# Kernel optimization log

Hardware: AMD Instinct MI355X
Metric: run time of the kernel (lower is better)

Reference implementation:

```python
import jax, jax.numpy as jnp
import numpy as np

B, NL, C, H, W = 4, 2048, 128, 128, 128
N_PTS0, N_PTS1 = 32, 8
SCALE = N_PTS0 // N_PTS1  # MaxPool1d kernel/stride
FEATURE_DIM = 5
BN_EPS = 1e-5


def setup_inputs() -> dict:
    key = jax.random.key(0)
    ks = jax.random.split(key, 12)
    fm = jax.random.normal(ks[0], (B, C, H, W), dtype=jnp.float32)
    lines = jax.random.uniform(ks[1], (B, NL, 2, 2), dtype=jnp.float32) * 128.0
    P = C // 2
    s = 0.05
    return {
        "feature_map": fm,
        "lines": lines,
        # Bottleneck1D params (BatchNorm in eval mode: running_mean=0, running_var=1)
        "bn1_g": jnp.ones((C,), jnp.float32), "bn1_b": jnp.zeros((C,), jnp.float32),
        "conv1_w": jax.random.normal(ks[2], (P, C, 1), jnp.float32) * s,
        "conv1_b": jnp.zeros((P,), jnp.float32),
        "bn2_g": jnp.ones((P,), jnp.float32), "bn2_b": jnp.zeros((P,), jnp.float32),
        "conv2_w": jax.random.normal(ks[3], (P, P, 3), jnp.float32) * s,
        "conv2_b": jnp.zeros((P,), jnp.float32),
        "bn3_g": jnp.ones((P,), jnp.float32), "bn3_b": jnp.zeros((P,), jnp.float32),
        "conv3_w": jax.random.normal(ks[4], (C, P, 1), jnp.float32) * s,
        "conv3_b": jnp.zeros((C,), jnp.float32),
        # fc2: ReLU -> Linear(dim_loi*n_pts1 + 5, 4)
        "fc2_w": jax.random.normal(ks[5], (4, C * N_PTS1 + FEATURE_DIM), jnp.float32) * s,
        "fc2_b": jnp.zeros((4,), jnp.float32),
    }


def _bn(x, g, b):
    # eval-mode BatchNorm1d with running_mean=0, running_var=1
    return x * (g / jnp.sqrt(1.0 + BN_EPS))[None, :, None] + b[None, :, None]


def _conv1d(x, w, b, pad):
    y = jax.lax.conv_general_dilated(x, w, (1,), [(pad, pad)],
                                     dimension_numbers=("NCH", "OIH", "NCH"))
    return y + b[None, :, None]


def _loi_gather(fm, lines):
    # sample points along each line: [B, NL, N_PTS0, 2]
    lam = jnp.linspace(0.0, 1.0, N_PTS0, dtype=jnp.float32)[None, None, :, None]
    p = lines[:, :, 0:1, :] * lam + lines[:, :, 1:2, :] * (1.0 - lam) - 0.5
    p = p.reshape(B, -1, 2)                      # [B, NL*N_PTS0, 2]
    px, py = p[..., 0], p[..., 1]
    px0 = jnp.clip(jnp.floor(px), 0.0, 127.0)
    py0 = jnp.clip(jnp.floor(py), 0.0, 127.0)
    px1 = jnp.clip(px0 + 1.0, 0.0, 127.0)
    py1 = jnp.clip(py0 + 1.0, 0.0, 127.0)
    px0l, py0l = px0.astype(jnp.int32), py0.astype(jnp.int32)
    px1l, py1l = px1.astype(jnp.int32), py1.astype(jnp.int32)

    gather = jax.vmap(lambda f, yi, xi: f[:, yi, xi])  # [C, P] per image
    # weights exactly as in the torch source
    xp = (gather(fm, py0l, px0l) * ((px1 - px) * (py1 - py))[:, None, :]
          + gather(fm, py1l, px0l) * ((px - px0) * (py1 - py))[:, None, :]
          + gather(fm, py0l, px1l) * ((px1 - px) * (py - py0))[:, None, :]
          + gather(fm, py1l, px1l) * ((px - px0) * (py - py0))[:, None, :])
    # [B, C, NL*N_PTS0] -> [B*NL, C, N_PTS0]
    xp = xp.reshape(B, C, NL, N_PTS0).transpose(0, 2, 1, 3).reshape(B * NL, C, N_PTS0)
    return xp


def reference(feature_map, lines, bn1_g, bn1_b, conv1_w, conv1_b,
              bn2_g, bn2_b, conv2_w, conv2_b, bn3_g, bn3_b,
              conv3_w, conv3_b, fc2_w, fc2_b):
    xp = _loi_gather(feature_map, lines)               # [B*NL, C, N_PTS0]
    # MaxPool1d(SCALE, SCALE)
    x = xp.reshape(B * NL, C, N_PTS1, SCALE).max(axis=-1)
    # Bottleneck1D residual block
    y = jax.nn.relu(_bn(x, bn1_g, bn1_b))
    y = _conv1d(y, conv1_w, conv1_b, 0)
    y = jax.nn.relu(_bn(y, bn2_g, bn2_b))
    y = _conv1d(y, conv2_w, conv2_b, 1)
    y = jax.nn.relu(_bn(y, bn3_g, bn3_b))
    y = _conv1d(y, conv3_w, conv3_b, 0)
    x = x + y                                          # [B*NL, C, N_PTS1]
    # line geometry feature (use_cood=1, use_slop=1)
    xyu, xyv = lines[:, :, 0, :], lines[:, :, 1, :]
    u2v = jnp.sqrt(((xyu - xyv) ** 2).sum(-1, keepdims=True)).clip(min=1e-6)
    f = jnp.concatenate([xyu / 128.0, xyv / 128.0, u2v], axis=-1)
    f = f.reshape(B * NL, FEATURE_DIM)
    # concat + fc2 (ReLU -> Linear)
    x = jnp.concatenate([x.reshape(B * NL, C * N_PTS1), f], axis=1)
    logits = jax.nn.relu(x) @ fc2_w.T + fc2_b
    prob = jax.nn.softmax(logits, axis=1)
    return logits, prob
```

## Files before the change

### kernel.cpp

```cpp
#include <hip/hip_runtime.h>
#include <math.h>

#define BB 4
#define NLL 2048
#define CC 128
#define HH 128
#define WW 128
#define NPTS0 32
#define NPTS1 8
#define PP 64
#define FDIM 5
#define FCK (CC*NPTS1 + FDIM)
#define FCKP 1032

typedef __attribute__((ext_vector_type(8))) short bf16x8;
typedef __attribute__((ext_vector_type(4))) float f32x4;

__device__ __forceinline__ unsigned short f2bf(float f) {
    union { float f; unsigned u; } v; v.f = f;
    unsigned u = v.u;
    return (unsigned short)((u + 0x7fffu + ((u >> 16) & 1u)) >> 16);
}
__device__ __forceinline__ float bf2f(unsigned short s) {
    union { unsigned u; float f; } v; v.u = ((unsigned)s) << 16;
    return v.f;
}

__global__ __launch_bounds__(256)
void transpose_prep(const float* __restrict__ fm, const float* __restrict__ w1,
                    const float* __restrict__ w2, const float* __restrict__ w3,
                    const float* __restrict__ fcw,
                    unsigned short* __restrict__ fmT,
                    unsigned short* __restrict__ W1b,
                    unsigned short* __restrict__ W2b,
                    unsigned short* __restrict__ W3b,
                    float* __restrict__ fcwP) {
    const int t = threadIdx.x;
    if (blockIdx.x >= 512) {
        int gid = (blockIdx.x - 512) * 256 + t;
        for (int e = gid; e < 32800; e += 4096) {
            if (e < 8192) {
                W1b[e] = f2bf(w1[e]);
            } else if (e < 20480) {
                int g = e - 8192;
                int tt = g >> 12, r = g & 4095;
                int p = r >> 6, q = r & 63;
                W2b[tt * 4096 + p * 64 + q] = f2bf(w2[p * 192 + q * 3 + tt]);
            } else if (e < 28672) {
                int g = e - 20480;
                W3b[g] = f2bf(w3[g]);
            } else {
                int g = e - 28672;
                int o = g / FCKP, r = g - o * FCKP;
                fcwP[g] = (r < FCK) ? fcw[o * FCK + r] : 0.0f;
            }
        }
        return;
    }
    __shared__ unsigned short tile[2][128 * 72];
    const int by = blockIdx.x;
    const int b = by >> 7, y = by & 127;
    const float* src = fm + ((size_t)b * CC) * (HH * WW) + (size_t)y * WW;
    const int x4 = (t & 31) * 4;
    const int xh = x4 >> 6, xl = x4 & 63;
    #pragma unroll
    for (int i = 0; i < 16; ++i) {
        int r = (t >> 5) + 8 * i;
        float4 v = *(const float4*)&src[(size_t)r * (HH * WW) + x4];
        ushort4 u;
        u.x = f2bf(v.x); u.y = f2bf(v.y); u.z = f2bf(v.z); u.w = f2bf(v.w);
        *(ushort4*)&tile[xh][r * 72 + (xl ^ (r & 28))] = u;
    }
    __syncthreads();
    const int c4 = (t & 31) * 4;
    #pragma unroll
    for (int h = 0; h < 2; ++h) {
        unsigned short* dst = fmT + ((size_t)by * WW + h * 64) * CC;
        #pragma unroll
        for (int i = 0; i < 8; ++i) {
            int x = (t >> 5) + 8 * i;
            ushort4 u;
            u.x = tile[h][(c4 + 0) * 72 + (x ^ ((c4 + 0) & 28))];
            u.y = tile[h][(c4 + 1) * 72 + (x ^ ((c4 + 1) & 28))];
            u.z = tile[h][(c4 + 2) * 72 + (x ^ ((c4 + 2) & 28))];
            u.w = tile[h][(c4 + 3) * 72 + (x ^ ((c4 + 3) & 28))];
            *(ushort4*)&dst[(size_t)x * CC + c4] = u;
        }
    }
}

__global__ __launch_bounds__(256, 8)
void line_mfma(const unsigned short* __restrict__ fmT,
               const float* __restrict__ lines,
               const float* __restrict__ bn1_g, const float* __restrict__ bn1_b,
               const unsigned short* __restrict__ W1b, const float* __restrict__ b1,
               const float* __restrict__ bn2_g, const float* __restrict__ bn2_b,
               const unsigned short* __restrict__ W2b, const float* __restrict__ b2,
               const float* __restrict__ bn3_g, const float* __restrict__ bn3_b,
               const unsigned short* __restrict__ W3b, const float* __restrict__ b3,
               const float* __restrict__ fcwP,  const float* __restrict__ fcb,
               float* __restrict__ out) {
    __shared__ int   s_oA[64], s_oB[64], s_oC[64], s_oD[64];
    __shared__ float s_wA[64], s_wB[64], s_wC[64], s_wD[64];
    __shared__ float s_xs[16 * 132];
    __shared__ unsigned short s_ybn[16 * 136];
    __shared__ unsigned short s_z1[2 * 10 * 72];
    __shared__ unsigned short s_z2[16 * 72];
    __shared__ float s_feat[2][8];
    __shared__ float s_red[4 * 8];

    const int bx  = blockIdx.x;
    const int L0  = bx * 2;
    const int b   = bx >> 10;
    const int tid = threadIdx.x;
    const int lane = tid & 63;
    const int wv   = tid >> 6;
    const int quad = lane >> 4;
    const int l16  = lane & 15;
    const float inv_s = 1.0f / sqrtf(1.0f + 1e-5f);

    if (tid < 64) {
        int line = tid >> 5, pt = tid & 31;
        const float* ln = lines + (size_t)(L0 + line) * 4;
        float lam = (float)pt * (1.0f / 31.0f);
        float om  = 1.0f - lam;
        float px = ln[0] * lam + ln[2] * om - 0.5f;
        float py = ln[1] * lam + ln[3] * om - 0.5f;
        float px0 = fminf(fmaxf(floorf(px), 0.0f), 127.0f);
        float py0 = fminf(fmaxf(floorf(py), 0.0f), 127.0f);
        float px1 = fminf(px0 + 1.0f, 127.0f);
        float py1 = fminf(py0 + 1.0f, 127.0f);
        int ix0 = (int)px0, ix1 = (int)px1, iy0 = (int)py0, iy1 = (int)py1;
        s_oA[tid] = (iy0 * WW + ix0) * CC;
        s_oB[tid] = (iy1 * WW + ix0) * CC;
        s_oC[tid] = (iy0 * WW + ix1) * CC;
        s_oD[tid] = (iy1 * WW + ix1) * CC;
        float ax = px1 - px, bxv = px - px0, ay = py1 - py, byv = py - py0;
        s_wA[tid] = ax  * ay;
        s_wB[tid] = bxv * ay;
        s_wC[tid] = ax  * byv;
        s_wD[tid] = bxv * byv;
    }
    if (tid >= 64 && tid < 66) {
        int line = tid - 64;
        const float* ln = lines + (size_t)(L0 + line) * 4;
        float ux = ln[0], uy = ln[1], vx = ln[2], vy = ln[3];
        float dx = ux - vx, dy = uy - vy;
        float d = fmaxf(sqrtf(dx * dx + dy * dy), 1e-6f);
        s_feat[line][0] = ux * (1.0f / 128.0f);
        s_feat[line][1] = uy * (1.0f / 128.0f);
        s_feat[line][2] = vx * (1.0f / 128.0f);
        s_feat[line][3] = vy * (1.0f / 128.0f);
        s_feat[line][4] = d;
    }
    if (tid < 128) {
        int line = tid >> 6, q = tid & 63;
        s_z1[line * 720 + 0 * 72 + q] = 0;
        s_z1[line * 720 + 9 * 72 + q] = 0;
    }
    __syncthreads();

    {
        int tl = tid >> 4;
        int line = tl >> 3, k = tl & 7;
        int c8 = (tid & 15) * 8;
        const unsigned short* base = fmT + (size_t)b * (HH * WW * CC) + c8;
        float acc[8];
        #pragma unroll
        for (int i = 0; i < 8; ++i) acc[i] = -INFINITY;
        #pragma unroll
        for (int j = 0; j < 4; ++j) {
            int pt = line * 32 + k * 4 + j;
            bf16x8 rA = *(const bf16x8*)(base + s_oA[pt]);
            bf16x8 rB = *(const bf16x8*)(base + s_oB[pt]);
            bf16x8 rC = *(const bf16x8*)(base + s_oC[pt]);
            bf16x8 rD = *(const bf16x8*)(base + s_oD[pt]);
            float wA = s_wA[pt], wB = s_wB[pt], wC = s_wC[pt], wD = s_wD[pt];
            #pragma unroll
            for (int i = 0; i < 8; ++i) {
                float v = wA * bf2f((unsigned short)rA[i])
                        + wB * bf2f((unsigned short)rB[i])
                        + wC * bf2f((unsigned short)rC[i])
                        + wD * bf2f((unsigned short)rD[i]);
                acc[i] = fmaxf(acc[i], v);
            }
        }
        float* xr = &s_xs[tl * 132 + c8];
        f32x4 lo = {acc[0], acc[1], acc[2], acc[3]};
        f32x4 hi = {acc[4], acc[5], acc[6], acc[7]};
        *(f32x4*)&xr[0] = lo;
        *(f32x4*)&xr[4] = hi;
        bf16x8 pack;
        #pragma unroll
        for (int i = 0; i < 8; ++i) {
            float v = fmaxf(acc[i] * (bn1_g[c8 + i] * inv_s) + bn1_b[c8 + i], 0.0f);
            pack[i] = (short)f2bf(v);
        }
        *(bf16x8*)&s_ybn[tl * 136 + c8] = pack;
    }
    __syncthreads();

    {
        int n0 = wv * 16;
        f32x4 acc = {0.f, 0.f, 0.f, 0.f};
        #pragma unroll
        for (int kc = 0; kc < 4; ++kc) {
            bf16x8 a = *(const bf16x8*)&s_ybn[l16 * 136 + kc * 32 + quad * 8];
            bf16x8 bf = *(const bf16x8*)(W1b + (n0 + l16) * 128 + kc * 32 + quad * 8);
            acc = __builtin_amdgcn_mfma_f32_16x16x32_bf16(a, bf, acc, 0, 0, 0);
        }
        int p = n0 + l16;
        float s2 = bn2_g[p] * inv_s, bb2 = bn2_b[p], cb = b1[p];
        int line = quad >> 1;
        int kbase = (quad & 1) * 4;
        #pragma unroll
        for (int r = 0; r < 4; ++r) {
            float v = fmaxf((acc[r] + cb) * s2 + bb2, 0.0f);
            s_z1[line * 720 + (kbase + r + 1) * 72 + p] = f2bf(v);
        }
    }
    __syncthreads();

    {
        int n0 = wv * 16;
        f32x4 acc = {0.f, 0.f, 0.f, 0.f};
        int line = l16 >> 3, k = l16 & 7;
        #pragma unroll
        for (int t = 0; t < 3; ++t) {
            const unsigned short* arow = &s_z1[line * 720 + (k + t) * 72];
            #pragma unroll
            for (int kc = 0; kc < 2; ++kc) {
                bf16x8 a = *(const bf16x8*)&arow[kc * 32 + quad * 8];
                bf16x8 bf = *(const bf16x8*)(W2b + t * 4096 + (n0 + l16) * 64 + kc * 32 + quad * 8);
                acc = __builtin_amdgcn_mfma_f32_16x16x32_bf16(a, bf, acc, 0, 0, 0);
            }
        }
        int p = n0 + l16;
        float s3 = bn3_g[p] * inv_s, bb3 = bn3_b[p], cb = b2[p];
        #pragma unroll
        for (int r = 0; r < 4; ++r) {
            float v = fmaxf((acc[r] + cb) * s3 + bb3, 0.0f);
            s_z2[(quad * 4 + r) * 72 + p] = f2bf(v);
        }
    }
    __syncthreads();

    float p0 = 0.f, p1 = 0.f, p2 = 0.f, p3 = 0.f;
    {
        int kbase = (quad & 1) * 4;
        bf16x8 a0 = *(const bf16x8*)&s_z2[l16 * 72 + 0 * 32 + quad * 8];
        bf16x8 a1 = *(const bf16x8*)&s_z2[l16 * 72 + 1 * 32 + quad * 8];
        #pragma unroll
        for (int sub = 0; sub < 2; ++sub) {
            int n0 = wv * 32 + sub * 16;
            f32x4 acc = {0.f, 0.f, 0.f, 0.f};
            bf16x8 bf0 = *(const bf16x8*)(W3b + (n0 + l16) * 64 + 0 * 32 + quad * 8);
            bf16x8 bf1 = *(const bf16x8*)(W3b + (n0 + l16) * 64 + 1 * 32 + quad * 8);
            acc = __builtin_amdgcn_mfma_f32_16x16x32_bf16(a0, bf0, acc, 0, 0, 0);
            acc = __builtin_amdgcn_mfma_f32_16x16x32_bf16(a1, bf1, acc, 0, 0, 0);
            int c = n0 + l16;
            float cb = b3[c];
            int idx = c * 8 + kbase;
            float4 w0 = *(const float4*)(fcwP + 0 * FCKP + idx);
            float4 w1v = *(const float4*)(fcwP + 1 * FCKP + idx);
            float4 w2v = *(const float4*)(fcwP + 2 * FCKP + idx);
            float4 w3v = *(const float4*)(fcwP + 3 * FCKP + idx);
            const float* w0a = (const float*)&w0;
            const float* w1a = (const float*)&w1v;
            const float* w2a = (const float*)&w2v;
            const float* w3a = (const float*)&w3v;
            #pragma unroll
            for (int r = 0; r < 4; ++r) {
                int m = quad * 4 + r;
                float v = fmaxf(s_xs[m * 132 + c] + acc[r] + cb, 0.0f);
                p0 = fmaf(v, w0a[r], p0);
                p1 = fmaf(v, w1a[r], p1);
                p2 = fmaf(v, w2a[r], p2);
                p3 = fmaf(v, w3a[r], p3);
            }
        }
    }
    #pragma unroll
    for (int off = 16; off >= 1; off >>= 1) {
        p0 += __shfl_down(p0, off);
        p1 += __shfl_down(p1, off);
        p2 += __shfl_down(p2, off);
        p3 += __shfl_down(p3, off);
    }
    if ((lane & 31) == 0) {
        int line = lane >> 5;
        s_red[wv * 8 + line * 4 + 0] = p0;
        s_red[wv * 8 + line * 4 + 1] = p1;
        s_red[wv * 8 + line * 4 + 2] = p2;
        s_red[wv * 8 + line * 4 + 3] = p3;
    }
    __syncthreads();

    if (tid < 2) {
        int line = tid;
        float lg[4];
        #pragma unroll
        for (int o = 0; o < 4; ++o) {
            lg[o] = fcb[o] + s_red[0 + line * 4 + o] + s_red[8 + line * 4 + o]
                  + s_red[16 + line * 4 + o] + s_red[24 + line * 4 + o];
        }
        #pragma unroll
        for (int j = 0; j < FDIM; ++j) {
            float fv = fmaxf(s_feat[line][j], 0.0f);
            #pragma unroll
            for (int o = 0; o < 4; ++o)
                lg[o] = fmaf(fv, fcwP[o * FCKP + 1024 + j], lg[o]);
        }
        float m = fmaxf(fmaxf(lg[0], lg[1]), fmaxf(lg[2], lg[3]));
        float e0 = expf(lg[0] - m), e1 = expf(lg[1] - m);
        float e2 = expf(lg[2] - m), e3 = expf(lg[3] - m);
        float inv = 1.0f / (e0 + e1 + e2 + e3);
        float* lo = out + (size_t)(L0 + line) * 4;
        lo[0] = lg[0]; lo[1] = lg[1]; lo[2] = lg[2]; lo[3] = lg[3];
        float* pr = out + (size_t)BB * NLL * 4 + (size_t)(L0 + line) * 4;
        pr[0] = e0 * inv; pr[1] = e1 * inv; pr[2] = e2 * inv; pr[3] = e3 * inv;
    }
}

__global__ __launch_bounds__(256)
void transpose_fm2(const float* __restrict__ fm, float* __restrict__ fmT) {
    __shared__ float tile[32 * 132];
    const int c0 = blockIdx.x * 32;
    const int by = blockIdx.y;
    const int b = by >> 7, y = by & 127;
    const int t = threadIdx.x;
    const float* src = fm + ((size_t)b * CC) * (HH * WW) + (size_t)y * WW;
    const int x4 = (t & 31) * 4;
    #pragma unroll
    for (int i = 0; i < 4; ++i) {
        int r = (t >> 5) + 8 * i;
        *(float4*)&tile[r * 132 + x4] =
            *(const float4*)&src[(size_t)(c0 + r) * (HH * WW) + x4];
    }
    __syncthreads();
    float* dst = fmT + (size_t)by * WW * CC + c0 + (t & 31);
    const int cr = (t & 31) * 132;
    #pragma unroll
    for (int i = 0; i < 16; ++i) {
        int x = (t >> 5) + 8 * i;
        dst[(size_t)x * CC] = tile[cr + x];
    }
}

template<bool TRANS>
__global__ __launch_bounds__(256)
void line_kernel_v1(const float* __restrict__ fm,
                    const float* __restrict__ lines,
                    const float* __restrict__ bn1_g, const float* __restrict__ bn1_b,
                    const float* __restrict__ w1,    const float* __restrict__ b1,
                    const float* __restrict__ bn2_g, const float* __restrict__ bn2_b,
                    const float* __restrict__ w2,    const float* __restrict__ b2,
                    const float* __restrict__ bn3_g, const float* __restrict__ bn3_b,
                    const float* __restrict__ w3,    const float* __restrict__ b3,
                    const float* __restrict__ fcw,   const float* __restrict__ fcb,
                    float* __restrict__ out) {
    __shared__ int   s_ix0[32], s_ix1[32], s_iy0[32], s_iy1[32];
    __shared__ float s_wA[32], s_wB[32], s_wC[32], s_wD[32];
    __shared__ float xs [8][132];
    __shared__ float ybn[8][132];
    __shared__ float z1 [64][12];
    __shared__ float z2 [64][8];
    __shared__ float s_feat[8];
    __shared__ float s_red[16];

    const int L   = blockIdx.x;
    const int b   = L / NLL;
    const int tid = threadIdx.x;
    const float inv_s = 1.0f / sqrtf(1.0f + 1e-5f);
    const float* ln = lines + (size_t)L * 4;

    if (tid < 32) {
        float lam = (float)tid * (1.0f / 31.0f);
        float om  = 1.0f - lam;
        float px = ln[0] * lam + ln[2] * om - 0.5f;
        float py = ln[1] * lam + ln[3] * om - 0.5f;
        float px0 = fminf(fmaxf(floorf(px), 0.0f), 127.0f);
        float py0 = fminf(fmaxf(floorf(py), 0.0f), 127.0f);
        float px1 = fminf(px0 + 1.0f, 127.0f);
        float py1 = fminf(py0 + 1.0f, 127.0f);
        s_ix0[tid] = (int)px0; s_ix1[tid] = (int)px1;
        s_iy0[tid] = (int)py0; s_iy1[tid] = (int)py1;
        float ax = px1 - px, bxv = px - px0, ay = py1 - py, byv = py - py0;
        s_wA[tid] = ax  * ay;  s_wB[tid] = bxv * ay;
        s_wC[tid] = ax  * byv; s_wD[tid] = bxv * byv;
    }
    if (tid == 0) {
        float ux = ln[0], uy = ln[1], vx = ln[2], vy = ln[3];
        float dx = ux - vx, dy = uy - vy;
        float d = fmaxf(sqrtf(dx * dx + dy * dy), 1e-6f);
        s_feat[0] = ux / 128.0f; s_feat[1] = uy / 128.0f;
        s_feat[2] = vx / 128.0f; s_feat[3] = vy / 128.0f;
        s_feat[4] = d;
    }
    __syncthreads();
    {
        int cq = tid & 31, k = tid >> 5, c0 = cq * 4;
        float4 acc;
        acc.x = -INFINITY; acc.y = -INFINITY; acc.z = -INFINITY; acc.w = -INFINITY;
        #pragma unroll
        for (int j = 0; j < 4; ++j) {
            int pt = k * 4 + j;
            int ix0 = s_ix0[pt], ix1 = s_ix1[pt];
            int iy0 = s_iy0[pt], iy1 = s_iy1[pt];
            float wA = s_wA[pt], wB = s_wB[pt], wC = s_wC[pt], wD = s_wD[pt];
            float4 vA, vB, vC, vD;
            if (TRANS) {
                const float* base = fm + (size_t)b * HH * WW * CC;
                vA = *(const float4*)(base + ((size_t)(iy0 * WW + ix0)) * CC + c0);
                vB = *(const float4*)(base + ((size_t)(iy1 * WW + ix0)) * CC + c0);
                vC = *(const float4*)(base + ((size_t)(iy0 * WW + ix1)) * CC + c0);
                vD = *(const float4*)(base + ((size_t)(iy1 * WW + ix1)) * CC + c0);
            } else {
                const float* base = fm + ((size_t)b * CC + c0) * HH * WW;
                int oA = iy0 * WW + ix0, oB = iy1 * WW + ix0;
                int oC = iy0 * WW + ix1, oD = iy1 * WW + ix1;
                vA.x = base[oA];           vB.x = base[oB];
                vC.x = base[oC];           vD.x = base[oD];
                vA.y = base[HH*WW + oA];   vB.y = base[HH*WW + oB];
                vC.y = base[HH*WW + oC];   vD.y = base[HH*WW + oD];
                vA.z = base[2*HH*WW + oA]; vB.z = base[2*HH*WW + oB];
                vC.z = base[2*HH*WW + oC]; vD.z = base[2*HH*WW + oD];
                vA.w = base[3*HH*WW + oA]; vB.w = base[3*HH*WW + oB];
                vC.w = base[3*HH*WW + oC]; vD.w = base[3*HH*WW + oD];
            }
            float4 v;
            v.x = wA * vA.x + wB * vB.x + wC * vC.x + wD * vD.x;
            v.y = wA * vA.y + wB * vB.y + wC * vC.y + wD * vD.y;
            v.z = wA * vA.z + wB * vB.z + wC * vC.z + wD * vD.z;
            v.w = wA * vA.w + wB * vB.w + wC * vC.w + wD * vD.w;
            acc.x = fmaxf(acc.x, v.x); acc.y = fmaxf(acc.y, v.y);
            acc.z = fmaxf(acc.z, v.z); acc.w = fmaxf(acc.w, v.w);
        }
        *(float4*)(&xs[k][c0]) = acc;
    }
    __syncthreads();
    for (int e = tid; e < 1024; e += 256) {
        int k = e >> 7, c = e & 127;
        ybn[k][c] = fmaxf(xs[k][c] * (bn1_g[c] * inv_s) + bn1_b[c], 0.0f);
    }
    __syncthreads();
    if (tid < 64) { z1[tid][0] = 0.0f; z1[tid][9] = 0.0f; }
    {
        int p = tid >> 2, kq = tid & 3;
        const float* wrow = w1 + p * 128;
        float a0a = 0.f, a0b = 0.f, a1a = 0.f, a1b = 0.f;
        #pragma unroll 8
        for (int c = 0; c < 128; c += 4) {
            float4 w  = *(const float4*)(wrow + c);
            float4 ya = *(const float4*)(&ybn[kq][c]);
            float4 yb = *(const float4*)(&ybn[kq + 4][c]);
            a0a = fmaf(w.x, ya.x, a0a); a0b = fmaf(w.y, ya.y, a0b);
            a0a = fmaf(w.z, ya.z, a0a); a0b = fmaf(w.w, ya.w, a0b);
            a1a = fmaf(w.x, yb.x, a1a); a1b = fmaf(w.y, yb.y, a1b);
            a1a = fmaf(w.z, yb.z, a1a); a1b = fmaf(w.w, yb.w, a1b);
        }
        float s2 = bn2_g[p] * inv_s, bb = bn2_b[p], cb = b1[p];
        z1[p][1 + kq]     = fmaxf((a0a + a0b + cb) * s2 + bb, 0.0f);
        z1[p][1 + kq + 4] = fmaxf((a1a + a1b + cb) * s2 + bb, 0.0f);
    }
    __syncthreads();
    {
        int p = tid >> 2, kq = tid & 3;
        const float* wrow = w2 + p * 192;
        float acc0 = 0.f, acc1 = 0.f;
        #pragma unroll 4
        for (int q = 0; q < 64; ++q) {
            float w0 = wrow[q * 3 + 0], w1v = wrow[q * 3 + 1], w2v = wrow[q * 3 + 2];
            const float* zr = &z1[q][0];
            acc0 = fmaf(w0, zr[kq], acc0);
            acc0 = fmaf(w1v, zr[kq + 1], acc0);
            acc0 = fmaf(w2v, zr[kq + 2], acc0);
            acc1 = fmaf(w0, zr[kq + 4], acc1);
            acc1 = fmaf(w1v, zr[kq + 5], acc1);
            acc1 = fmaf(w2v, zr[kq + 6], acc1);
        }
        float s3 = bn3_g[p] * inv_s, bb = bn3_b[p], cb = b2[p];
        z2[p][kq]     = fmaxf((acc0 + cb) * s3 + bb, 0.0f);
        z2[p][kq + 4] = fmaxf((acc1 + cb) * s3 + bb, 0.0f);
    }
    __syncthreads();
    float part0 = 0.f, part1 = 0.f, part2 = 0.f, part3 = 0.f;
    {
        int c = tid >> 1, kq = tid & 1;
        const float* wrow = w3 + c * 64;
        float acc[4] = {0.f, 0.f, 0.f, 0.f};
        #pragma unroll 8
        for (int q = 0; q < 64; ++q) {
            float w = wrow[q];
            acc[0] = fmaf(w, z2[q][kq], acc[0]);
            acc[1] = fmaf(w, z2[q][kq + 2], acc[1]);
            acc[2] = fmaf(w, z2[q][kq + 4], acc[2]);
            acc[3] = fmaf(w, z2[q][kq + 6], acc[3]);
        }
        float cb = b3[c];
        #pragma unroll
        for (int i = 0; i < 4; ++i) {
            int k = kq + 2 * i;
            float v = fmaxf(xs[k][c] + acc[i] + cb, 0.0f);
            int idx = c * 8 + k;
            part0 = fmaf(v, fcw[0 * FCK + idx], part0);
            part1 = fmaf(v, fcw[1 * FCK + idx], part1);
            part2 = fmaf(v, fcw[2 * FCK + idx], part2);
            part3 = fmaf(v, fcw[3 * FCK + idx], part3);
        }
    }
    #pragma unroll
    for (int off = 32; off > 0; off >>= 1) {
        part0 += __shfl_down(part0, off);
        part1 += __shfl_down(part1, off);
        part2 += __shfl_down(part2, off);
        part3 += __shfl_down(part3, off);
    }
    if ((tid & 63) == 0) {
        int w = tid >> 6;
        s_red[w * 4 + 0] = part0; s_red[w * 4 + 1] = part1;
        s_red[w * 4 + 2] = part2; s_red[w * 4 + 3] = part3;
    }
    __syncthreads();
    if (tid == 0) {
        float lg[4];
        #pragma unroll
        for (int o = 0; o < 4; ++o)
            lg[o] = fcb[o] + s_red[o] + s_red[4 + o] + s_red[8 + o] + s_red[12 + o];
        #pragma unroll
        for (int j = 0; j < FDIM; ++j) {
            float fv = fmaxf(s_feat[j], 0.0f);
            #pragma unroll
            for (int o = 0; o < 4; ++o)
                lg[o] = fmaf(fv, fcw[o * FCK + 1024 + j], lg[o]);
        }
        float m = fmaxf(fmaxf(lg[0], lg[1]), fmaxf(lg[2], lg[3]));
        float e0 = expf(lg[0] - m), e1 = expf(lg[1] - m);
        float e2 = expf(lg[2] - m), e3 = expf(lg[3] - m);
        float inv = 1.0f / (e0 + e1 + e2 + e3);
        float* lo = out + (size_t)L * 4;
        lo[0] = lg[0]; lo[1] = lg[1]; lo[2] = lg[2]; lo[3] = lg[3];
        float* pr = out + (size_t)BB * NLL * 4 + (size_t)L * 4;
        pr[0] = e0 * inv; pr[1] = e1 * inv; pr[2] = e2 * inv; pr[3] = e3 * inv;
    }
}

extern "C" void kernel_launch(void* const* d_in, const int* in_sizes, int n_in,
                              void* d_out, int out_size, void* d_ws, size_t ws_size,
                              hipStream_t stream) {
    const float* fm     = (const float*)d_in[0];
    const float* lines  = (const float*)d_in[1];
    const float* bn1_g  = (const float*)d_in[2];
    const float* bn1_b  = (const float*)d_in[3];
    const float* w1     = (const float*)d_in[4];
    const float* b1     = (const float*)d_in[5];
    const float* bn2_g  = (const float*)d_in[6];
    const float* bn2_b  = (const float*)d_in[7];
    const float* w2     = (const float*)d_in[8];
    const float* b2     = (const float*)d_in[9];
    const float* bn3_g  = (const float*)d_in[10];
    const float* bn3_b  = (const float*)d_in[11];
    const float* w3     = (const float*)d_in[12];
    const float* b3     = (const float*)d_in[13];
    const float* fcw    = (const float*)d_in[14];
    const float* fcb    = (const float*)d_in[15];
    float* out = (float*)d_out;

    const size_t fmTb_bytes = (size_t)BB * HH * WW * CC * sizeof(unsigned short);
    const size_t fmTf_bytes = (size_t)BB * HH * WW * CC * sizeof(float);
    const size_t wb_bytes   = 57344;
    const size_t fcwP_bytes = 4 * FCKP * sizeof(float);

    if (ws_size >= fmTb_bytes + wb_bytes + fcwP_bytes) {
        unsigned short* fmT = (unsigned short*)d_ws;
        unsigned short* W1b = (unsigned short*)((char*)d_ws + fmTb_bytes);
        unsigned short* W2b = W1b + 8192;
        unsigned short* W3b = W2b + 12288;
        float* fcwP = (float*)((char*)d_ws + fmTb_bytes + wb_bytes);
        transpose_prep<<<512 + 16, 256, 0, stream>>>(
            fm, w1, w2, w3, fcw, fmT, W1b, W2b, W3b, fcwP);
        line_mfma<<<BB * NLL / 2, 256, 0, stream>>>(
            fmT, lines, bn1_g, bn1_b, W1b, b1, bn2_g, bn2_b, W2b, b2,
            bn3_g, bn3_b, W3b, b3, fcwP, fcb, out);
    } else if (ws_size >= fmTf_bytes) {
        float* fmT = (float*)d_ws;
        dim3 tg(CC / 32, BB * HH);
        transpose_fm2<<<tg, 256, 0, stream>>>(fm, fmT);
        line_kernel_v1<true><<<BB * NLL, 256, 0, stream>>>(
            fmT, lines, bn1_g, bn1_b, w1, b1, bn2_g, bn2_b, w2, b2,
            bn3_g, bn3_b, w3, b3, fcw, fcb, out);
    } else {
        line_kernel_v1<false><<<BB * NLL, 256, 0, stream>>>(
            fm, lines, bn1_g, bn1_b, w1, b1, bn2_g, bn2_b, w2, b2,
            bn3_g, bn3_b, w3, b3, fcw, fcb, out);
    }
}
```

Before: 149.8 us.

## Process four lines per block with fused in-register bilinear coordinate computation

Each block now handles four lines instead of two, so the MFMA M dimension becomes 32 rows and each wave reuses its loaded A fragments across two N subtiles, halving the block count. Sample coordinates and weights are computed per thread in registers rather than staged through shared memory, which removes one barrier. The pooled activations are stored as bf16 with BN1 applied during the MFMA A-load, and geometry features are computed in the final step. In exchange, per-thread gather width doubles to 16 channels, register pressure rises (launch bound lowered to 6), and the residual path now uses bf16-rounded values.

```diff
diff --git a/kernel.cpp b/kernel.cpp
--- a/kernel.cpp
+++ b/kernel.cpp
@@ -89,7 +89,7 @@
     }
 }
 
-__global__ __launch_bounds__(256, 8)
+__global__ __launch_bounds__(256, 6)
 void line_mfma(const unsigned short* __restrict__ fmT,
                const float* __restrict__ lines,
                const float* __restrict__ bn1_g, const float* __restrict__ bn1_b,
@@ -100,18 +100,14 @@
                const unsigned short* __restrict__ W3b, const float* __restrict__ b3,
                const float* __restrict__ fcwP,  const float* __restrict__ fcb,
                float* __restrict__ out) {
-    __shared__ int   s_oA[64], s_oB[64], s_oC[64], s_oD[64];
-    __shared__ float s_wA[64], s_wB[64], s_wC[64], s_wD[64];
-    __shared__ float s_xs[16 * 132];
-    __shared__ unsigned short s_ybn[16 * 136];
-    __shared__ unsigned short s_z1[2 * 10 * 72];
-    __shared__ unsigned short s_z2[16 * 72];
-    __shared__ float s_feat[2][8];
+    __shared__ unsigned short s_xs[32 * 136];
+    __shared__ unsigned short s_z1[4 * 10 * 72];
+    __shared__ unsigned short s_z2[32 * 72];
     __shared__ float s_red[4 * 8];
 
     const int bx  = blockIdx.x;
-    const int L0  = bx * 2;
-    const int b   = bx >> 10;
+    const int L0  = bx * 4;
+    const int b   = bx >> 9;
     const int tid = threadIdx.x;
     const int lane = tid & 63;
     const int wv   = tid >> 6;
@@ -119,146 +115,165 @@
     const int l16  = lane & 15;
     const float inv_s = 1.0f / sqrtf(1.0f + 1e-5f);
 
-    if (tid < 64) {
-        int line = tid >> 5, pt = tid & 31;
+    {
+        int m = tid >> 3;
+        int line = m >> 3, k = m & 7;
+        int c16 = (tid & 7) * 16;
         const float* ln = lines + (size_t)(L0 + line) * 4;
-        float lam = (float)pt * (1.0f / 31.0f);
-        float om  = 1.0f - lam;
-        float px = ln[0] * lam + ln[2] * om - 0.5f;
-        float py = ln[1] * lam + ln[3] * om - 0.5f;
-        float px0 = fminf(fmaxf(floorf(px), 0.0f), 127.0f);
-        float py0 = fminf(fmaxf(floorf(py), 0.0f), 127.0f);
-        float px1 = fminf(px0 + 1.0f, 127.0f);
-        float py1 = fminf(py0 + 1.0f, 127.0f);
-        int ix0 = (int)px0, ix1 = (int)px1, iy0 = (int)py0, iy1 = (int)py1;
-        s_oA[tid] = (iy0 * WW + ix0) * CC;
-        s_oB[tid] = (iy1 * WW + ix0) * CC;
-        s_oC[tid] = (iy0 * WW + ix1) * CC;
-        s_oD[tid] = (iy1 * WW + ix1) * CC;
-        float ax = px1 - px, bxv = px - px0, ay = py1 - py, byv = py - py0;
-        s_wA[tid] = ax  * ay;
-        s_wB[tid] = bxv * ay;
-        s_wC[tid] = ax  * byv;
-        s_wD[tid] = bxv * byv;
-    }
-    if (tid >= 64 && tid < 66) {
-        int line = tid - 64;
-        const float* ln = lines + (size_t)(L0 + line) * 4;
-        float ux = ln[0], uy = ln[1], vx = ln[2], vy = ln[3];
-        float dx = ux - vx, dy = uy - vy;
-        float d = fmaxf(sqrtf(dx * dx + dy * dy), 1e-6f);
-        s_feat[line][0] = ux * (1.0f / 128.0f);
-        s_feat[line][1] = uy * (1.0f / 128.0f);
-        s_feat[line][2] = vx * (1.0f / 128.0f);
-        s_feat[line][3] = vy * (1.0f / 128.0f);
-        s_feat[line][4] = d;
-    }
-    if (tid < 128) {
-        int line = tid >> 6, q = tid & 63;
-        s_z1[line * 720 + 0 * 72 + q] = 0;
-        s_z1[line * 720 + 9 * 72 + q] = 0;
-    }
-    __syncthreads();
-
-    {
-        int tl = tid >> 4;
-        int line = tl >> 3, k = tl & 7;
-        int c8 = (tid & 15) * 8;
-        const unsigned short* base = fmT + (size_t)b * (HH * WW * CC) + c8;
-        float acc[8];
-        #pragma unroll
-        for (int i = 0; i < 8; ++i) acc[i] = -INFINITY;
+        float lx0 = ln[0], ly0 = ln[1], lx1 = ln[2], ly1 = ln[3];
+        const unsigned short* base = fmT + (size_t)b * (HH * WW * CC) + c16;
+        float acc[16];
+        #pragma unroll
+        for (int i = 0; i < 16; ++i) acc[i] = -INFINITY;
         #pragma unroll
         for (int j = 0; j < 4; ++j) {
-            int pt = line * 32 + k * 4 + j;
-            bf16x8 rA = *(const bf16x8*)(base + s_oA[pt]);
-            bf16x8 rB = *(const bf16x8*)(base + s_oB[pt]);
-            bf16x8 rC = *(const bf16x8*)(base + s_oC[pt]);
-            bf16x8 rD = *(const bf16x8*)(base + s_oD[pt]);
-            float wA = s_wA[pt], wB = s_wB[pt], wC = s_wC[pt], wD = s_wD[pt];
+            int pt = k * 4 + j;
+            float lam = (float)pt * (1.0f / 31.0f);
+            float om  = 1.0f - lam;
+            float px = lx0 * lam + lx1 * om - 0.5f;
+            float py = ly0 * lam + ly1 * om - 0.5f;
+            float px0 = fminf(fmaxf(floorf(px), 0.0f), 127.0f);
+            float py0 = fminf(fmaxf(floorf(py), 0.0f), 127.0f);
+            float px1 = fminf(px0 + 1.0f, 127.0f);
+            float py1 = fminf(py0 + 1.0f, 127.0f);
+            int ix0 = (int)px0, ix1 = (int)px1, iy0 = (int)py0, iy1 = (int)py1;
+            float ax = px1 - px, bxv = px - px0, ay = py1 - py, byv = py - py0;
+            float wA = ax * ay, wB = bxv * ay, wC = ax * byv, wD = bxv * byv;
+            int oA = (iy0 * WW + ix0) * CC, oB = (iy1 * WW + ix0) * CC;
+            int oC = (iy0 * WW + ix1) * CC, oD = (iy1 * WW + ix1) * CC;
+            bf16x8 a0 = *(const bf16x8*)(base + oA);
+            bf16x8 a1 = *(const bf16x8*)(base + oA + 8);
+            bf16x8 b0 = *(const bf16x8*)(base + oB);
+            bf16x8 b1v = *(const bf16x8*)(base + oB + 8);
+            bf16x8 c0 = *(const bf16x8*)(base + oC);
+            bf16x8 c1 = *(const bf16x8*)(base + oC + 8);
+            bf16x8 d0 = *(const bf16x8*)(base + oD);
+            bf16x8 d1 = *(const bf16x8*)(base + oD + 8);
             #pragma unroll
             for (int i = 0; i < 8; ++i) {
-                float v = wA * bf2f((unsigned short)rA[i])
-                        + wB * bf2f((unsigned short)rB[i])
-                        + wC * bf2f((unsigned short)rC[i])
-                        + wD * bf2f((unsigned short)rD[i]);
+                float v = wA * bf2f((unsigned short)a0[i])
+                        + wB * bf2f((unsigned short)b0[i])
+                        + wC * bf2f((unsigned short)c0[i])
+                        + wD * bf2f((unsigned short)d0[i]);
                 acc[i] = fmaxf(acc[i], v);
-            }
-        }
-        float* xr = &s_xs[tl * 132 + c8];
-        f32x4 lo = {acc[0], acc[1], acc[2], acc[3]};
-        f32x4 hi = {acc[4], acc[5], acc[6], acc[7]};
-        *(f32x4*)&xr[0] = lo;
-        *(f32x4*)&xr[4] = hi;
-        bf16x8 pack;
+                float v2 = wA * bf2f((unsigned short)a1[i])
+                         + wB * bf2f((unsigned short)b1v[i])
+                         + wC * bf2f((unsigned short)c1[i])
+                         + wD * bf2f((unsigned short)d1[i]);
+                acc[8 + i] = fmaxf(acc[8 + i], v2);
+            }
+        }
+        bf16x8 lo, hi;
         #pragma unroll
         for (int i = 0; i < 8; ++i) {
-            float v = fmaxf(acc[i] * (bn1_g[c8 + i] * inv_s) + bn1_b[c8 + i], 0.0f);
-            pack[i] = (short)f2bf(v);
-        }
-        *(bf16x8*)&s_ybn[tl * 136 + c8] = pack;
-    }
-    __syncthreads();
-
-    {
-        int n0 = wv * 16;
-        f32x4 acc = {0.f, 0.f, 0.f, 0.f};
+            lo[i] = (short)f2bf(acc[i]);
+            hi[i] = (short)f2bf(acc[8 + i]);
+        }
+        *(bf16x8*)&s_xs[m * 136 + c16]     = lo;
+        *(bf16x8*)&s_xs[m * 136 + c16 + 8] = hi;
+    }
+    __syncthreads();
+
+    {
+        int mh = wv & 1, nh = wv >> 1;
+        int mrow = mh * 16 + l16;
+        bf16x8 afr[4];
         #pragma unroll
         for (int kc = 0; kc < 4; ++kc) {
-            bf16x8 a = *(const bf16x8*)&s_ybn[l16 * 136 + kc * 32 + quad * 8];
-            bf16x8 bf = *(const bf16x8*)(W1b + (n0 + l16) * 128 + kc * 32 + quad * 8);
-            acc = __builtin_amdgcn_mfma_f32_16x16x32_bf16(a, bf, acc, 0, 0, 0);
-        }
-        int p = n0 + l16;
-        float s2 = bn2_g[p] * inv_s, bb2 = bn2_b[p], cb = b1[p];
-        int line = quad >> 1;
+            bf16x8 x = *(const bf16x8*)&s_xs[mrow * 136 + kc * 32 + quad * 8];
+            int c0 = kc * 32 + quad * 8;
+            float4 g0 = *(const float4*)(bn1_g + c0);
+            float4 g1 = *(const float4*)(bn1_g + c0 + 4);
+            float4 bb0 = *(const float4*)(bn1_b + c0);
+            float4 bb1 = *(const float4*)(bn1_b + c0 + 4);
+            float gs[8] = {g0.x, g0.y, g0.z, g0.w, g1.x, g1.y, g1.z, g1.w};
+            float bs[8] = {bb0.x, bb0.y, bb0.z, bb0.w, bb1.x, bb1.y, bb1.z, bb1.w};
+            bf16x8 pk;
+            #pragma unroll
+            for (int i = 0; i < 8; ++i) {
+                float v = fmaxf(bf2f((unsigned short)x[i]) * (gs[i] * inv_s) + bs[i], 0.0f);
+                pk[i] = (short)f2bf(v);
+            }
+            afr[kc] = pk;
+        }
+        #pragma unroll
+        for (int sub = 0; sub < 2; ++sub) {
+            int p = nh * 32 + sub * 16 + l16;
+            f32x4 acc = {0.f, 0.f, 0.f, 0.f};
+            #pragma unroll
+            for (int kc = 0; kc < 4; ++kc) {
+                bf16x8 bf = *(const bf16x8*)(W1b + p * 128 + kc * 32 + quad * 8);
+                acc = __builtin_amdgcn_mfma_f32_16x16x32_bf16(afr[kc], bf, acc, 0, 0, 0);
+            }
+            float s2 = bn2_g[p] * inv_s, bb2 = bn2_b[p], cb = b1[p];
+            #pragma unroll
+            for (int r = 0; r < 4; ++r) {
+                int mm = mh * 16 + quad * 4 + r;
+                int lline = mm >> 3, kk = mm & 7;
+                float v = fmaxf((acc[r] + cb) * s2 + bb2, 0.0f);
+                s_z1[lline * 720 + (kk + 1) * 72 + p] = f2bf(v);
+            }
+        }
+        #pragma unroll
+        for (int e = tid; e < 512; e += 256) {
+            int lline = e >> 7;
+            int rr = (e >> 6) & 1;
+            int q = e & 63;
+            s_z1[lline * 720 + (rr ? 9 : 0) * 72 + q] = 0;
+        }
+    }
+    __syncthreads();
+
+    {
+        int mh = wv & 1, nh = wv >> 1;
+        int mrow = mh * 16 + l16;
+        int linea = mrow >> 3, ka = mrow & 7;
+        const unsigned short* arow = s_z1 + linea * 720 + ka * 72;
+        bf16x8 afr[3][2];
+        #pragma unroll
+        for (int t = 0; t < 3; ++t)
+            #pragma unroll
+            for (int kc = 0; kc < 2; ++kc)
+                afr[t][kc] = *(const bf16x8*)&arow[t * 72 + kc * 32 + quad * 8];
+        #pragma unroll
+        for (int sub = 0; sub < 2; ++sub) {
+            int p = nh * 32 + sub * 16 + l16;
+            f32x4 acc = {0.f, 0.f, 0.f, 0.f};
+            #pragma unroll
+            for (int t = 0; t < 3; ++t) {
+                #pragma unroll
+                for (int kc = 0; kc < 2; ++kc) {
+                    bf16x8 bf = *(const bf16x8*)(W2b + t * 4096 + p * 64 + kc * 32 + quad * 8);
+                    acc = __builtin_amdgcn_mfma_f32_16x16x32_bf16(afr[t][kc], bf, acc, 0, 0, 0);
+                }
+            }
+            float s3 = bn3_g[p] * inv_s, bb3 = bn3_b[p], cb = b2[p];
+            #pragma unroll
+            for (int r = 0; r < 4; ++r) {
+                int mm = mh * 16 + quad * 4 + r;
+                float v = fmaxf((acc[r] + cb) * s3 + bb3, 0.0f);
+                s_z2[mm * 72 + p] = f2bf(v);
+            }
+        }
+    }
+    __syncthreads();
+
+    float p0 = 0.f, p1 = 0.f, p2 = 0.f, p3 = 0.f;
+    {
+        int mh = wv & 1;
+        int n0 = (wv >> 1) * 64;
+        int mrow = mh * 16 + l16;
+        bf16x8 a0 = *(const bf16x8*)&s_z2[mrow * 72 + quad * 8];
+        bf16x8 a1 = *(const bf16x8*)&s_z2[mrow * 72 + 32 + quad * 8];
         int kbase = (quad & 1) * 4;
         #pragma unroll
-        for (int r = 0; r < 4; ++r) {
-            float v = fmaxf((acc[r] + cb) * s2 + bb2, 0.0f);
-            s_z1[line * 720 + (kbase + r + 1) * 72 + p] = f2bf(v);
-        }
-    }
-    __syncthreads();
-
-    {
-        int n0 = wv * 16;
-        f32x4 acc = {0.f, 0.f, 0.f, 0.f};
-        int line = l16 >> 3, k = l16 & 7;
-        #pragma unroll
-        for (int t = 0; t < 3; ++t) {
-            const unsigned short* arow = &s_z1[line * 720 + (k + t) * 72];
-            #pragma unroll
-            for (int kc = 0; kc < 2; ++kc) {
-                bf16x8 a = *(const bf16x8*)&arow[kc * 32 + quad * 8];
-                bf16x8 bf = *(const bf16x8*)(W2b + t * 4096 + (n0 + l16) * 64 + kc * 32 + quad * 8);
-                acc = __builtin_amdgcn_mfma_f32_16x16x32_bf16(a, bf, acc, 0, 0, 0);
-            }
-        }
-        int p = n0 + l16;
-        float s3 = bn3_g[p] * inv_s, bb3 = bn3_b[p], cb = b2[p];
-        #pragma unroll
-        for (int r = 0; r < 4; ++r) {
-            float v = fmaxf((acc[r] + cb) * s3 + bb3, 0.0f);
-            s_z2[(quad * 4 + r) * 72 + p] = f2bf(v);
-        }
-    }
-    __syncthreads();
-
-    float p0 = 0.f, p1 = 0.f, p2 = 0.f, p3 = 0.f;
-    {
-        int kbase = (quad & 1) * 4;
-        bf16x8 a0 = *(const bf16x8*)&s_z2[l16 * 72 + 0 * 32 + quad * 8];
-        bf16x8 a1 = *(const bf16x8*)&s_z2[l16 * 72 + 1 * 32 + quad * 8];
-        #pragma unroll
-        for (int sub = 0; sub < 2; ++sub) {
-            int n0 = wv * 32 + sub * 16;
+        for (int sub = 0; sub < 4; ++sub) {
+            int c = n0 + sub * 16 + l16;
             f32x4 acc = {0.f, 0.f, 0.f, 0.f};
-            bf16x8 bf0 = *(const bf16x8*)(W3b + (n0 + l16) * 64 + 0 * 32 + quad * 8);
-            bf16x8 bf1 = *(const bf16x8*)(W3b + (n0 + l16) * 64 + 1 * 32 + quad * 8);
+            bf16x8 bf0 = *(const bf16x8*)(W3b + c * 64 + quad * 8);
+            bf16x8 bf1 = *(const bf16x8*)(W3b + c * 64 + 32 + quad * 8);
             acc = __builtin_amdgcn_mfma_f32_16x16x32_bf16(a0, bf0, acc, 0, 0, 0);
             acc = __builtin_amdgcn_mfma_f32_16x16x32_bf16(a1, bf1, acc, 0, 0, 0);
-            int c = n0 + l16;
             float cb = b3[c];
             int idx = c * 8 + kbase;
             float4 w0 = *(const float4*)(fcwP + 0 * FCKP + idx);
@@ -271,8 +286,9 @@
             const float* w3a = (const float*)&w3v;
             #pragma unroll
             for (int r = 0; r < 4; ++r) {
-                int m = quad * 4 + r;
-                float v = fmaxf(s_xs[m * 132 + c] + acc[r] + cb, 0.0f);
+                int mm = mh * 16 + quad * 4 + r;
+                float xv = bf2f(s_xs[mm * 136 + c]);
+                float v = fmaxf(xv + acc[r] + cb, 0.0f);
                 p0 = fmaf(v, w0a[r], p0);
                 p1 = fmaf(v, w1a[r], p1);
                 p2 = fmaf(v, w2a[r], p2);
@@ -288,25 +304,31 @@
         p3 += __shfl_down(p3, off);
     }
     if ((lane & 31) == 0) {
-        int line = lane >> 5;
-        s_red[wv * 8 + line * 4 + 0] = p0;
-        s_red[wv * 8 + line * 4 + 1] = p1;
-        s_red[wv * 8 + line * 4 + 2] = p2;
-        s_red[wv * 8 + line * 4 + 3] = p3;
-    }
-    __syncthreads();
-
-    if (tid < 2) {
+        int h = lane >> 5;
+        s_red[wv * 8 + h * 4 + 0] = p0;
+        s_red[wv * 8 + h * 4 + 1] = p1;
+        s_red[wv * 8 + h * 4 + 2] = p2;
+        s_red[wv * 8 + h * 4 + 3] = p3;
+    }
+    __syncthreads();
+
+    if (tid < 4) {
         int line = tid;
+        int wa = line >> 1;
+        int h  = (line & 1) * 4;
         float lg[4];
         #pragma unroll
-        for (int o = 0; o < 4; ++o) {
-            lg[o] = fcb[o] + s_red[0 + line * 4 + o] + s_red[8 + line * 4 + o]
-                  + s_red[16 + line * 4 + o] + s_red[24 + line * 4 + o];
-        }
+        for (int o = 0; o < 4; ++o)
+            lg[o] = fcb[o] + s_red[wa * 8 + h + o] + s_red[(wa + 2) * 8 + h + o];
+        const float* ln = lines + (size_t)(L0 + line) * 4;
+        float ux = ln[0], uy = ln[1], vx = ln[2], vy = ln[3];
+        float dx = ux - vx, dy = uy - vy;
+        float d = fmaxf(sqrtf(dx * dx + dy * dy), 1e-6f);
+        float ft[FDIM] = {ux * (1.0f / 128.0f), uy * (1.0f / 128.0f),
+                          vx * (1.0f / 128.0f), vy * (1.0f / 128.0f), d};
         #pragma unroll
         for (int j = 0; j < FDIM; ++j) {
-            float fv = fmaxf(s_feat[line][j], 0.0f);
+            float fv = fmaxf(ft[j], 0.0f);
             #pragma unroll
             for (int o = 0; o < 4; ++o)
                 lg[o] = fmaf(fv, fcwP[o * FCKP + 1024 + j], lg[o]);
@@ -579,7 +601,7 @@
         float* fcwP = (float*)((char*)d_ws + fmTb_bytes + wb_bytes);
         transpose_prep<<<512 + 16, 256, 0, stream>>>(
             fm, w1, w2, w3, fcw, fmT, W1b, W2b, W3b, fcwP);
-        line_mfma<<<BB * NLL / 2, 256, 0, stream>>>(
+        line_mfma<<<BB * NLL / 4, 256, 0, stream>>>(
             fmT, lines, bn1_g, bn1_b, W1b, b1, bn2_g, bn2_b, W2b, b2,
             bn3_g, bn3_b, W3b, b3, fcwP, fcb, out);
     } else if (ws_size >= fmTf_bytes) {
```

After: 177.1 us. 18.3% more time.
